# Kernel optimization log

Hardware: AMD Instinct MI355X
Metric: run time of the kernel (lower is better)

The kernel has to match this reference:

```python
import jax, jax.numpy as jnp
from jax import lax
import numpy as np


def hac_round(X, W):
    """Avg-linkage HAC build+cut rounding of fractional SDP matrix X (D,D).
    Returns the 0/1 symmetric round_matrix with 1-diagonal."""
    D = X.shape[0]
    dt = X.dtype
    MAXD = jnp.max(jnp.abs(X)) * 1000.0  # _MAX_DIST sentinel
    max_sim = jnp.max(X)                 # max_similarity passed by forward()
    tril_mask = jnp.tril(jnp.ones((D, D), dtype=bool))
    # use_similarities=True branch: Y = MAXD*tril + (max_sim - X).triu(1)
    Y = jnp.where(tril_mask, MAXD, max_sim - X)
    values = jnp.min(Y, axis=1)
    indices = jnp.argmin(Y, axis=1)
    parents = jnp.arange(2 * D - 1)
    p2i = jnp.arange(2 * D - 1)   # parent_to_idx
    i2p = jnp.arange(D)           # idx_to_parent
    cs = jnp.ones(2 * D - 1, dtype=dt)
    energy = jnp.zeros(2 * D - 1, dtype=dt)
    clustering = jnp.zeros((2 * D - 1, D), dtype=dt)
    clustering = clustering.at[jnp.arange(D), jnp.arange(D)].set(jnp.arange(1, D + 1, dtype=dt))
    R = jnp.eye(D, dtype=dt)

    def body(i, st):
        Y, values, indices, parents, p2i, i2p, cs, energy, clustering, R = st
        max_node = D + i
        m1 = jnp.argmin(values)
        m2 = indices[m1]
        p1 = i2p[p2i[i2p[m1]]]
        p2 = i2p[p2i[i2p[m2]]]
        parents = parents.at[p1].set(max_node).at[p2].set(max_node)
        i2p = i2p.at[m1].set(max_node)
        p2i = p2i.at[max_node].set(m1)
        max_mask = Y == MAXD
        cs1, cs2 = cs[p1], cs[p2]
        ncs = cs1 + cs2
        cs = cs.at[max_node].set(ncs)
        # weighted average-linkage merged distances
        newv = (jnp.minimum(Y[m1, :], Y[:, m1]) * cs1 + jnp.minimum(Y[:, m2], Y[m2, :]) * cs2) / ncs
        Y = Y.at[:, m1].set(newv).at[m1, :].set(newv)
        Y = jnp.where(max_mask, MAXD, Y)
        Y = Y.at[:, m2].set(MAXD).at[m2, :].set(MAXD)
        values = values.at[m2].set(MAXD)
        vmask = values == MAXD
        values = jnp.where(vmask, MAXD, jnp.min(Y, axis=1))
        indices = jnp.argmin(Y, axis=1)
        # cut decision for the new internal node
        crow = clustering[p1] + clustering[p2]
        leaf = crow > 0                      # membership of new cluster
        lf = leaf.astype(dt)
        merge_e = lf @ (W @ lf)              # sum of W over leaf x leaf pairs
        e_sum = energy[p1] + energy[p2]
        take = merge_e >= e_sum
        energy = energy.at[max_node].set(jnp.where(take, merge_e, e_sum))
        crow = jnp.where(take & leaf, (max_node).astype(dt), crow)
        clustering = clustering.at[max_node].set(crow)
        R = jnp.where(take & (leaf[:, None] & leaf[None, :]), jnp.asarray(1.0, dt), R)
        return (Y, values, indices, parents, p2i, i2p, cs, energy, clustering, R)

    st = (Y, values, indices, parents, p2i, i2p, cs, energy, clustering, R)
    st = lax.fori_loop(0, D - 1, body, st)
    return st[-1]


def setup_inputs() -> dict:
    key = jax.random.key(0)
    k1, k2 = jax.random.split(key)
    D = 1024
    A = jax.random.uniform(k1, (D, D), dtype=jnp.float32)
    X = 0.5 * (A + A.T)                      # symmetric fractional decisions
    X = X.at[jnp.arange(D), jnp.arange(D)].set(1.0)  # 1-diagonal
    W = jnp.triu(jax.random.normal(k2, (D, D), dtype=jnp.float32), 1)  # triu(1) weights
    return {"X": X, "W": W}


def reference(X, W):
    # straight-through estimator: hard rounded solution, identity gradient w.r.t. X
    R = hac_round(X, W)
    return X + lax.stop_gradient(R - X)
```

## Files before the change

### kernel.cpp

```cpp
#include <hip/hip_runtime.h>
#include <stdint.h>

#define D 1024

typedef unsigned long long u64;
typedef unsigned int u32;

__device__ __forceinline__ u32 enc_f(float f) {
    u32 b = __float_as_uint(f);
    return (b & 0x80000000u) ? ~b : (b | 0x80000000u);
}
__device__ __forceinline__ float dec_f(u32 u) {
    u32 b = (u & 0x80000000u) ? (u ^ 0x80000000u) : ~u;
    return __uint_as_float(b);
}

__device__ __forceinline__ void barrier_lds_only() {
    __builtin_amdgcn_sched_barrier(0);
    asm volatile("s_waitcnt lgkmcnt(0)" ::: "memory");
    __builtin_amdgcn_s_barrier();
    asm volatile("" ::: "memory");
    __builtin_amdgcn_sched_barrier(0);
}

__global__ void k_maxred(const float* __restrict__ X, u32* scal) {
    float mx = -INFINITY, ma = 0.f;
    int stride = gridDim.x * blockDim.x;
    for (int i = blockIdx.x * blockDim.x + threadIdx.x; i < D * D; i += stride) {
        float v = X[i];
        mx = fmaxf(mx, v);
        ma = fmaxf(ma, fabsf(v));
    }
    for (int o = 32; o; o >>= 1) {
        mx = fmaxf(mx, __shfl_xor(mx, o));
        ma = fmaxf(ma, __shfl_xor(ma, o));
    }
    if ((threadIdx.x & 63) == 0) {
        atomicMax(&scal[0], enc_f(mx));
        atomicMax(&scal[1], enc_f(ma));
    }
}

__global__ void k_init(const float* __restrict__ X, const float* __restrict__ W,
                       float2* __restrict__ dc, const u32* __restrict__ scal) {
    int idx = blockIdx.x * blockDim.x + threadIdx.x;
    if (idx >= D * D) return;
    float max_sim = dec_f(scal[0]);
    float MAXD = __fmul_rn(dec_f(scal[1]), 1000.0f);
    int i = idx >> 10, j = idx & (D - 1);
    float x = X[idx];
    float di = (i == j) ? MAXD : __fsub_rn(max_sim, x);
    float cx = (i == j) ? 0.0f : (W[idx] + W[j * D + i]);
    dc[idx] = make_float2(di, cx);
}

__global__ void k_rowmin(const float2* __restrict__ dc, float* __restrict__ values_g,
                         int* __restrict__ indices_g, const u32* __restrict__ scal) {
    int r = blockIdx.x;
    int lane = threadIdx.x;
    float MAXD = __fmul_rn(dec_f(scal[1]), 1000.0f);
    u64 best = ((u64)__float_as_uint(MAXD) << 32);
    const float4* row4 = (const float4*)(dc + (size_t)r * D);
    for (int c = lane; c < D / 2; c += 64) {
        float4 q = row4[c];
        int j0 = c << 1;
        if (j0 > r) {
            u64 k = ((u64)__float_as_uint(q.x) << 32) | (u32)j0;
            if (k < best) best = k;
        }
        if (j0 + 1 > r) {
            u64 k = ((u64)__float_as_uint(q.z) << 32) | (u32)(j0 + 1);
            if (k < best) best = k;
        }
    }
    for (int o = 32; o; o >>= 1) {
        u64 k2 = __shfl_xor(best, o);
        if (k2 < best) best = k2;
    }
    if (lane == 0) {
        values_g[r] = __uint_as_float((u32)(best >> 32));
        indices_g[r] = (int)(best & 0xffffffffu);
    }
}

__global__ void __launch_bounds__(1024) k_hac(
        float2* __restrict__ dc,
        const float* __restrict__ values_g, const int* __restrict__ indices_g,
        int* __restrict__ labels_g, const u32* __restrict__ scal) {
    __shared__ __align__(16) float values_l[D];
    __shared__ float values_stage[D];
    __shared__ int indices_l[D];
    __shared__ __align__(16) float newv_l[D];
    __shared__ float cs_l[D];
    __shared__ unsigned char dead_l[D];
    __shared__ unsigned char marked_l[D];
    __shared__ int slot_l[D];
    __shared__ int label_l[D];
    __shared__ double within_l[D];
    __shared__ double energy_l[D];
    __shared__ int rlist[2][D];
    __shared__ int nrec[2];
    __shared__ u64 s_best[2];
    __shared__ float s_cross12;
    __shared__ int s_takeP, s_m1P, s_labP;

    const int t = threadIdx.x;
    const int lane = t & 63, wid = t >> 6;
    const float MAXD = __fmul_rn(dec_f(scal[1]), 1000.0f);
    const u32 MAXDb = __float_as_uint(MAXD);

    values_l[t] = values_g[t];
    indices_l[t] = indices_g[t];
    cs_l[t] = 1.0f;
    dead_l[t] = 0;
    marked_l[t] = 0;
    slot_l[t] = t;
    label_l[t] = t;
    within_l[t] = 0.0;
    energy_l[t] = 0.0;
    if (t == 0) {
        s_takeP = 0; s_m1P = -1; s_labP = 0;
        nrec[0] = 0; nrec[1] = 0;
        s_best[0] = ~0ull; s_best[1] = ~0ull;
    }
    __syncthreads();
    {
        u64 key = ((u64)__float_as_uint(values_l[t]) << 32) | ((u32)t << 10) |
                  (u32)indices_l[t];
        for (int o = 32; o; o >>= 1) {
            u64 k2 = __shfl_xor(key, o);
            if (k2 < key) key = k2;
        }
        if (lane == 0) atomicMin(&s_best[0], key);
    }
    __syncthreads();

    float pf0 = 0.f, pf1 = 0.f, pf2 = 0.f, pf3 = 0.f;

    for (int it = 0; it < D - 1; ++it) {
        const int cb = it & 1, pb = cb ^ 1;

        const u64 bk = s_best[cb];
        const int m1 = (int)((bk >> 10) & 1023);
        const int m2 = (int)(bk & 1023);

        const float2 v1 = dc[(size_t)m1 * D + t];
        const float2 v2 = dc[(size_t)m2 * D + t];

        const float cs1 = cs_l[m1], cs2 = cs_l[m2];
        const float v_std = values_l[t];
        const float v_stg = values_stage[t];
        const int mk = marked_l[t];
        const int dd = dead_l[t];
        int idx = indices_l[t];
        const int sl = slot_l[t];
        const int pm1 = s_m1P;
        const int takeP = s_takeP, labP = s_labP;
        if (t == 0) s_best[pb] = ~0ull;

        const float ncs = __fadd_rn(cs1, cs2);

        float v = mk ? v_stg : v_std;
        if (mk) { values_l[t] = v; marked_l[t] = 0; }
        if (t == m2) {
            dead_l[m2] = 1;
            values_l[m2] = MAXD;
            indices_l[m2] = 0;
            v = MAXD;
            idx = 0;
        }
        const bool alive = !dd && (t != m2);

        const float d1 = v1.x, c1 = v1.y, d2 = v2.x, c2 = v2.y;

        if (takeP && sl == pm1) label_l[t] = labP;
        if (sl == m2) slot_l[t] = m1;

        float nv = MAXD, ncx = 0.0f;
        bool do_st = false;
        if (t == m2) s_cross12 = c1;
        if (alive && t != m1) {
            nv = __fdiv_rn(__fadd_rn(__fmul_rn(d1, cs1), __fmul_rn(d2, cs2)), ncs);
            ncx = c1 + c2;
            dc[(size_t)m1 * D + t] = make_float2(nv, ncx);
            do_st = true;
        }
        newv_l[t] = nv;

        if (t == m1) {
            values_l[t] = MAXD;
            marked_l[t] = 1;
        } else if (alive && v < MAXD) {
            if (idx == m2) {
                rlist[cb][atomicAdd(&nrec[cb], 1)] = t;
                values_l[t] = MAXD;
                marked_l[t] = 1;
            } else if (idx == m1) {
                if (nv <= v) values_l[t] = nv;
                else {
                    rlist[cb][atomicAdd(&nrec[cb], 1)] = t;
                    values_l[t] = MAXD;
                    marked_l[t] = 1;
                }
            } else if (t < m1) {
                if (nv < v) { values_l[t] = nv; indices_l[t] = m1; }
                else if (nv == v && m1 < idx) indices_l[t] = m1;
            }
        }
        barrier_lds_only();

        if (t == m1) cs_l[m1] = ncs;
        const int n = nrec[cb];
        if (t == 0) nrec[pb] = 0;

        if (wid == 0) {
            if (do_st) dc[(size_t)t * D + m1] = make_float2(nv, ncx);
            if (lane == 0) {
                double merge_e = within_l[m1] + within_l[m2] + (double)s_cross12;
                double e_sum = energy_l[m1] + energy_l[m2];
                int take = (merge_e >= e_sum) ? 1 : 0;
                within_l[m1] = merge_e;
                energy_l[m1] = take ? merge_e : e_sum;
                s_takeP = take;
                s_m1P = m1;
                s_labP = D + it;
            }
            const float4* v4 = (const float4*)values_l;
            u64 bb = ~0ull;
#pragma unroll
            for (int c = 0; c < 4; ++c) {
                int fi = lane + 64 * c;
                float4 q = v4[fi];
                int b = fi << 2;
                u64 k;
                k = ((u64)__float_as_uint(q.x) << 32) | (u32)(b + 0); if (k < bb) bb = k;
                k = ((u64)__float_as_uint(q.y) << 32) | (u32)(b + 1); if (k < bb) bb = k;
                k = ((u64)__float_as_uint(q.z) << 32) | (u32)(b + 2); if (k < bb) bb = k;
                k = ((u64)__float_as_uint(q.w) << 32) | (u32)(b + 3); if (k < bb) bb = k;
            }
            for (int o = 32; o; o >>= 1) {
                u64 k2 = __shfl_xor(bb, o);
                if (k2 < bb) bb = k2;
            }
            if (lane == 0) {
                int r = (int)(bb & 1023);
                int idx2 = indices_l[r];
                atomicMin(&s_best[pb],
                          (bb & 0xffffffff00000000ull) | ((u32)r << 10) | (u32)idx2);
            }
            {
                int r_pf = (int)(bb & 1023);
                int i_pf = indices_l[r_pf];
                const float* br = (const float*)(dc + (size_t)r_pf * D);
                const float* bi = (const float*)(dc + (size_t)i_pf * D);
                pf0 = br[lane * 16];
                pf1 = br[1024 + lane * 16];
                pf2 = bi[lane * 16];
                pf3 = bi[1024 + lane * 16];
            }
        } else if (wid == 1) {
            if (do_st) dc[(size_t)t * D + m1] = make_float2(nv, ncx);
            u64 bb = ((u64)MAXDb << 32);
            const float4* nv4 = (const float4*)newv_l;
            for (int c = lane; c < D / 4; c += 64) {
                float4 q = nv4[c];
                int j0 = c << 2;
#pragma unroll
                for (int e = 0; e < 4; ++e) {
                    int j = j0 + e;
                    float dv = (e == 0) ? q.x : (e == 1) ? q.y : (e == 2) ? q.z : q.w;
                    if (j > m1) {
                        u64 k = ((u64)__float_as_uint(dv) << 32) | (u32)j;
                        if (k < bb) bb = k;
                    }
                }
            }
            for (int o = 32; o; o >>= 1) {
                u64 k2 = __shfl_xor(bb, o);
                if (k2 < bb) bb = k2;
            }
            if (lane == 0) {
                values_stage[m1] = __uint_as_float((u32)(bb >> 32));
                indices_l[m1] = (int)(bb & 0xffffffffu);
                atomicMin(&s_best[pb],
                          (bb & 0xffffffff00000000ull) | ((u32)m1 << 10) | (bb & 1023));
            }
        } else {
            bool pend_st = do_st;
            for (int q = wid - 2; q < n; q += 14) {
                const int r = rlist[cb][q];
                const float subst = newv_l[r];
                const float4* row4 = (const float4*)(dc + (size_t)r * D);
                const int c0 = r >> 1;
                int ci0 = c0 + lane;       if (ci0 > 511) ci0 = 511;
                int ci1 = c0 + lane + 64;  if (ci1 > 511) ci1 = 511;
                int ci2 = c0 + lane + 128; if (ci2 > 511) ci2 = 511;
                int ci3 = c0 + lane + 192; if (ci3 > 511) ci3 = 511;
                int ci4 = c0 + lane + 256; if (ci4 > 511) ci4 = 511;
                int ci5 = c0 + lane + 320; if (ci5 > 511) ci5 = 511;
                int ci6 = c0 + lane + 384; if (ci6 > 511) ci6 = 511;
                int ci7 = c0 + lane + 448; if (ci7 > 511) ci7 = 511;
                float4 a0 = row4[ci0];
                float4 a1 = row4[ci1];
                float4 a2 = row4[ci2];
                float4 a3 = row4[ci3];
                float4 a4 = row4[ci4];
                float4 a5 = row4[ci5];
                float4 a6 = row4[ci6];
                float4 a7 = row4[ci7];
                if (pend_st) {
                    dc[(size_t)t * D + m1] = make_float2(nv, ncx);
                    pend_st = false;
                }
                u64 bb = ((u64)MAXDb << 32);
#define ACC2(af, civ)                                                           \
                {                                                               \
                    int j0 = (civ) << 1;                                        \
                    float dv0 = (j0 == m1) ? subst : (af).x;                    \
                    if (j0 > r && !dead_l[j0]) {                                \
                        u64 k = ((u64)__float_as_uint(dv0) << 32) | (u32)j0;    \
                        if (k < bb) bb = k;                                     \
                    }                                                           \
                    int j1 = j0 + 1;                                            \
                    float dv1 = (j1 == m1) ? subst : (af).z;                    \
                    if (j1 > r && !dead_l[j1]) {                                \
                        u64 k = ((u64)__float_as_uint(dv1) << 32) | (u32)j1;    \
                        if (k < bb) bb = k;                                     \
                    }                                                           \
                }
                ACC2(a0, ci0)
                ACC2(a1, ci1)
                ACC2(a2, ci2)
                ACC2(a3, ci3)
                ACC2(a4, ci4)
                ACC2(a5, ci5)
                ACC2(a6, ci6)
                ACC2(a7, ci7)
#undef ACC2
                for (int o = 32; o; o >>= 1) {
                    u64 k2 = __shfl_xor(bb, o);
                    if (k2 < bb) bb = k2;
                }
                if (lane == 0) {
                    values_stage[r] = __uint_as_float((u32)(bb >> 32));
                    indices_l[r] = (int)(bb & 0xffffffffu);
                    atomicMin(&s_best[pb],
                              (bb & 0xffffffff00000000ull) | ((u32)r << 10) | (bb & 1023));
                }
            }
            if (pend_st) dc[(size_t)t * D + m1] = make_float2(nv, ncx);
        }
        __syncthreads();
        if (wid == 0) asm volatile("" :: "v"(pf0), "v"(pf1), "v"(pf2), "v"(pf3));
    }

    {
        int lab = label_l[t];
        if (s_takeP && slot_l[t] == s_m1P) lab = s_labP;
        labels_g[t] = lab;
    }
}

__global__ void k_out(const int* __restrict__ labels, float* __restrict__ out) {
    int idx = blockIdx.x * blockDim.x + threadIdx.x;
    if (idx >= D * D) return;
    int i = idx >> 10, j = idx & (D - 1);
    out[idx] = (i == j || labels[i] == labels[j]) ? 1.0f : 0.0f;
}

extern "C" void kernel_launch(void* const* d_in, const int* in_sizes, int n_in,
                              void* d_out, int out_size, void* d_ws, size_t ws_size,
                              hipStream_t stream) {
    const float* X = (const float*)d_in[0];
    const float* W = (const float*)d_in[1];

    char* ws = (char*)d_ws;
    const size_t MAT_BYTES = (size_t)D * D * sizeof(float);
    float2* dc = (float2*)ws;
    float* values_g = (float*)(ws + 2 * MAT_BYTES);
    int* indices_g = (int*)(ws + 2 * MAT_BYTES + 4096);
    int* labels_g = (int*)(ws + 2 * MAT_BYTES + 8192);
    u32* scal = (u32*)(ws + 2 * MAT_BYTES + 12288);

    hipMemsetAsync(scal, 0, 2 * sizeof(u32), stream);
    k_maxred<<<256, 256, 0, stream>>>(X, scal);
    k_init<<<(D * D) / 256, 256, 0, stream>>>(X, W, dc, scal);
    k_rowmin<<<D, 64, 0, stream>>>(dc, values_g, indices_g, scal);
    k_hac<<<1, 1024, 0, stream>>>(dc, values_g, indices_g, labels_g, scal);
    k_out<<<(D * D) / 256, 256, 0, stream>>>(labels_g, (float*)d_out);
}
```

Measured before the change: 3.084 ms.

## Offload merged-row global stores to dedicated waves, forwarding values via LDS

Waves 0-7 now each process two columns of the merge update, and waves 8-15 do all the global writes of the merged row and column. The previous iteration's new row is double-buffered in LDS (newv_h/crossv_h), and readers of row m1/m2 take values from it when they touch the just-merged cluster. This lets the end-of-iteration `__syncthreads` become an LDS-only barrier, so store latency leaves the serial critical path. The cost is that row rescans now run on 6 waves instead of 14, and correctness depends on the store-visibility forwarding being exact.

```diff
diff --git a/kernel.cpp b/kernel.cpp
--- a/kernel.cpp
+++ b/kernel.cpp
@@ -90,7 +90,8 @@
     __shared__ __align__(16) float values_l[D];
     __shared__ float values_stage[D];
     __shared__ int indices_l[D];
-    __shared__ __align__(16) float newv_l[D];
+    __shared__ __align__(16) float newv_h[2][D];
+    __shared__ __align__(16) float crossv_h[2][D];
     __shared__ float cs_l[D];
     __shared__ unsigned char dead_l[D];
     __shared__ unsigned char marked_l[D];
@@ -143,214 +144,263 @@
         const u64 bk = s_best[cb];
         const int m1 = (int)((bk >> 10) & 1023);
         const int m2 = (int)(bk & 1023);
-
-        const float2 v1 = dc[(size_t)m1 * D + t];
-        const float2 v2 = dc[(size_t)m2 * D + t];
-
-        const float cs1 = cs_l[m1], cs2 = cs_l[m2];
-        const float v_std = values_l[t];
-        const float v_stg = values_stage[t];
-        const int mk = marked_l[t];
-        const int dd = dead_l[t];
-        int idx = indices_l[t];
-        const int sl = slot_l[t];
-        const int pm1 = s_m1P;
-        const int takeP = s_takeP, labP = s_labP;
-        if (t == 0) s_best[pb] = ~0ull;
-
-        const float ncs = __fadd_rn(cs1, cs2);
-
-        float v = mk ? v_stg : v_std;
-        if (mk) { values_l[t] = v; marked_l[t] = 0; }
-        if (t == m2) {
-            dead_l[m2] = 1;
-            values_l[m2] = MAXD;
-            indices_l[m2] = 0;
-            v = MAXD;
-            idx = 0;
-        }
-        const bool alive = !dd && (t != m2);
-
-        const float d1 = v1.x, c1 = v1.y, d2 = v2.x, c2 = v2.y;
-
-        if (takeP && sl == pm1) label_l[t] = labP;
-        if (sl == m2) slot_l[t] = m1;
-
-        float nv = MAXD, ncx = 0.0f;
-        bool do_st = false;
-        if (t == m2) s_cross12 = c1;
-        if (alive && t != m1) {
-            nv = __fdiv_rn(__fadd_rn(__fmul_rn(d1, cs1), __fmul_rn(d2, cs2)), ncs);
-            ncx = c1 + c2;
-            dc[(size_t)m1 * D + t] = make_float2(nv, ncx);
-            do_st = true;
-        }
-        newv_l[t] = nv;
-
-        if (t == m1) {
-            values_l[t] = MAXD;
-            marked_l[t] = 1;
-        } else if (alive && v < MAXD) {
-            if (idx == m2) {
-                rlist[cb][atomicAdd(&nrec[cb], 1)] = t;
-                values_l[t] = MAXD;
-                marked_l[t] = 1;
-            } else if (idx == m1) {
-                if (nv <= v) values_l[t] = nv;
-                else {
-                    rlist[cb][atomicAdd(&nrec[cb], 1)] = t;
-                    values_l[t] = MAXD;
-                    marked_l[t] = 1;
-                }
-            } else if (t < m1) {
-                if (nv < v) { values_l[t] = nv; indices_l[t] = m1; }
-                else if (nv == v && m1 < idx) indices_l[t] = m1;
-            }
+        const int c0 = (wid < 8) ? t : (t - 512);
+        const int c1 = c0 + 512;
+        float ncs = 0.f;
+
+        if (wid < 8) {
+            const float2 v1a = dc[(size_t)m1 * D + c0];
+            const float2 v1b = dc[(size_t)m1 * D + c1];
+            const float2 v2a = dc[(size_t)m2 * D + c0];
+            const float2 v2b = dc[(size_t)m2 * D + c1];
+
+            const int pm1 = s_m1P;
+            const float cs1 = cs_l[m1], cs2 = cs_l[m2];
+            float va = values_l[c0], vb = values_l[c1];
+            const float sga = values_stage[c0], sgb = values_stage[c1];
+            const int mka = marked_l[c0], mkb = marked_l[c1];
+            const int dda = dead_l[c0], ddb = dead_l[c1];
+            int ia = indices_l[c0], ib = indices_l[c1];
+            const int sla = slot_l[c0], slb = slot_l[c1];
+            const int takeP = s_takeP, labP = s_labP;
+            if (t == 0) s_best[pb] = ~0ull;
+
+            ncs = __fadd_rn(cs1, cs2);
+            const bool h1 = (m1 == pm1), h2 = (m2 == pm1);
+
+            if (mka) { va = sga; values_l[c0] = va; marked_l[c0] = 0; }
+            if (mkb) { vb = sgb; values_l[c1] = vb; marked_l[c1] = 0; }
+            if (c0 == m2) { dead_l[m2] = 1; values_l[m2] = MAXD; indices_l[m2] = 0; va = MAXD; ia = 0; }
+            if (c1 == m2) { dead_l[m2] = 1; values_l[m2] = MAXD; indices_l[m2] = 0; vb = MAXD; ib = 0; }
+            const bool alA = !dda && (c0 != m2);
+            const bool alB = !ddb && (c1 != m2);
+
+            float d1a = v1a.x, x1a = v1a.y, d1b = v1b.x, x1b = v1b.y;
+            float d2a = v2a.x, x2a = v2a.y, d2b = v2b.x, x2b = v2b.y;
+            if (h1) {
+                d1a = newv_h[pb][c0]; x1a = crossv_h[pb][c0];
+                d1b = newv_h[pb][c1]; x1b = crossv_h[pb][c1];
+            } else {
+                if (c0 == pm1) { d1a = newv_h[pb][m1]; x1a = crossv_h[pb][m1]; }
+                if (c1 == pm1) { d1b = newv_h[pb][m1]; x1b = crossv_h[pb][m1]; }
+            }
+            if (h2) {
+                d2a = newv_h[pb][c0]; x2a = crossv_h[pb][c0];
+                d2b = newv_h[pb][c1]; x2b = crossv_h[pb][c1];
+            } else {
+                if (c0 == pm1) { d2a = newv_h[pb][m2]; x2a = crossv_h[pb][m2]; }
+                if (c1 == pm1) { d2b = newv_h[pb][m2]; x2b = crossv_h[pb][m2]; }
+            }
+
+            if (takeP && sla == pm1) label_l[c0] = labP;
+            if (takeP && slb == pm1) label_l[c1] = labP;
+            if (sla == m2) slot_l[c0] = m1;
+            if (slb == m2) slot_l[c1] = m1;
+
+            if (c0 == m2) s_cross12 = x1a;
+            if (c1 == m2) s_cross12 = x1b;
+
+            float nva = MAXD, nxa = 0.0f, nvb = MAXD, nxb = 0.0f;
+            if (alA && c0 != m1) {
+                nva = __fdiv_rn(__fadd_rn(__fmul_rn(d1a, cs1), __fmul_rn(d2a, cs2)), ncs);
+                nxa = x1a + x2a;
+            }
+            if (alB && c1 != m1) {
+                nvb = __fdiv_rn(__fadd_rn(__fmul_rn(d1b, cs1), __fmul_rn(d2b, cs2)), ncs);
+                nxb = x1b + x2b;
+            }
+            newv_h[cb][c0] = nva; crossv_h[cb][c0] = nxa;
+            newv_h[cb][c1] = nvb; crossv_h[cb][c1] = nxb;
+
+            if (c0 == m1) {
+                values_l[c0] = MAXD;
+                marked_l[c0] = 1;
+            } else if (alA && va < MAXD) {
+                if (ia == m2) {
+                    rlist[cb][atomicAdd(&nrec[cb], 1)] = c0;
+                    values_l[c0] = MAXD; marked_l[c0] = 1;
+                } else if (ia == m1) {
+                    if (nva <= va) values_l[c0] = nva;
+                    else {
+                        rlist[cb][atomicAdd(&nrec[cb], 1)] = c0;
+                        values_l[c0] = MAXD; marked_l[c0] = 1;
+                    }
+                } else if (c0 < m1) {
+                    if (nva < va) { values_l[c0] = nva; indices_l[c0] = m1; }
+                    else if (nva == va && m1 < ia) indices_l[c0] = m1;
+                }
+            }
+            if (c1 == m1) {
+                values_l[c1] = MAXD;
+                marked_l[c1] = 1;
+            } else if (alB && vb < MAXD) {
+                if (ib == m2) {
+                    rlist[cb][atomicAdd(&nrec[cb], 1)] = c1;
+                    values_l[c1] = MAXD; marked_l[c1] = 1;
+                } else if (ib == m1) {
+                    if (nvb <= vb) values_l[c1] = nvb;
+                    else {
+                        rlist[cb][atomicAdd(&nrec[cb], 1)] = c1;
+                        values_l[c1] = MAXD; marked_l[c1] = 1;
+                    }
+                } else if (c1 < m1) {
+                    if (nvb < vb) { values_l[c1] = nvb; indices_l[c1] = m1; }
+                    else if (nvb == vb && m1 < ib) indices_l[c1] = m1;
+                }
+            }
+        } else {
+            asm volatile("s_waitcnt vmcnt(0)" ::: "memory");
         }
         barrier_lds_only();
 
-        if (t == m1) cs_l[m1] = ncs;
         const int n = nrec[cb];
         if (t == 0) nrec[pb] = 0;
 
-        if (wid == 0) {
-            if (do_st) dc[(size_t)t * D + m1] = make_float2(nv, ncx);
-            if (lane == 0) {
-                double merge_e = within_l[m1] + within_l[m2] + (double)s_cross12;
-                double e_sum = energy_l[m1] + energy_l[m2];
-                int take = (merge_e >= e_sum) ? 1 : 0;
-                within_l[m1] = merge_e;
-                energy_l[m1] = take ? merge_e : e_sum;
-                s_takeP = take;
-                s_m1P = m1;
-                s_labP = D + it;
-            }
-            const float4* v4 = (const float4*)values_l;
-            u64 bb = ~0ull;
+        if (wid < 8) {
+            if (c0 == m1 || c1 == m1) cs_l[m1] = ncs;
+
+            if (wid == 0) {
+                if (lane == 0) {
+                    double merge_e = within_l[m1] + within_l[m2] + (double)s_cross12;
+                    double e_sum = energy_l[m1] + energy_l[m2];
+                    int take = (merge_e >= e_sum) ? 1 : 0;
+                    within_l[m1] = merge_e;
+                    energy_l[m1] = take ? merge_e : e_sum;
+                    s_takeP = take;
+                    s_m1P = m1;
+                    s_labP = D + it;
+                }
+                const float4* v4 = (const float4*)values_l;
+                u64 bb = ~0ull;
 #pragma unroll
-            for (int c = 0; c < 4; ++c) {
-                int fi = lane + 64 * c;
-                float4 q = v4[fi];
-                int b = fi << 2;
-                u64 k;
-                k = ((u64)__float_as_uint(q.x) << 32) | (u32)(b + 0); if (k < bb) bb = k;
-                k = ((u64)__float_as_uint(q.y) << 32) | (u32)(b + 1); if (k < bb) bb = k;
-                k = ((u64)__float_as_uint(q.z) << 32) | (u32)(b + 2); if (k < bb) bb = k;
-                k = ((u64)__float_as_uint(q.w) << 32) | (u32)(b + 3); if (k < bb) bb = k;
-            }
-            for (int o = 32; o; o >>= 1) {
-                u64 k2 = __shfl_xor(bb, o);
-                if (k2 < bb) bb = k2;
-            }
-            if (lane == 0) {
-                int r = (int)(bb & 1023);
-                int idx2 = indices_l[r];
-                atomicMin(&s_best[pb],
-                          (bb & 0xffffffff00000000ull) | ((u32)r << 10) | (u32)idx2);
-            }
-            {
-                int r_pf = (int)(bb & 1023);
-                int i_pf = indices_l[r_pf];
-                const float* br = (const float*)(dc + (size_t)r_pf * D);
-                const float* bi = (const float*)(dc + (size_t)i_pf * D);
-                pf0 = br[lane * 16];
-                pf1 = br[1024 + lane * 16];
-                pf2 = bi[lane * 16];
-                pf3 = bi[1024 + lane * 16];
-            }
-        } else if (wid == 1) {
-            if (do_st) dc[(size_t)t * D + m1] = make_float2(nv, ncx);
-            u64 bb = ((u64)MAXDb << 32);
-            const float4* nv4 = (const float4*)newv_l;
-            for (int c = lane; c < D / 4; c += 64) {
-                float4 q = nv4[c];
-                int j0 = c << 2;
-#pragma unroll
-                for (int e = 0; e < 4; ++e) {
-                    int j = j0 + e;
-                    float dv = (e == 0) ? q.x : (e == 1) ? q.y : (e == 2) ? q.z : q.w;
-                    if (j > m1) {
-                        u64 k = ((u64)__float_as_uint(dv) << 32) | (u32)j;
-                        if (k < bb) bb = k;
-                    }
-                }
-            }
-            for (int o = 32; o; o >>= 1) {
-                u64 k2 = __shfl_xor(bb, o);
-                if (k2 < bb) bb = k2;
-            }
-            if (lane == 0) {
-                values_stage[m1] = __uint_as_float((u32)(bb >> 32));
-                indices_l[m1] = (int)(bb & 0xffffffffu);
-                atomicMin(&s_best[pb],
-                          (bb & 0xffffffff00000000ull) | ((u32)m1 << 10) | (bb & 1023));
-            }
-        } else {
-            bool pend_st = do_st;
-            for (int q = wid - 2; q < n; q += 14) {
-                const int r = rlist[cb][q];
-                const float subst = newv_l[r];
-                const float4* row4 = (const float4*)(dc + (size_t)r * D);
-                const int c0 = r >> 1;
-                int ci0 = c0 + lane;       if (ci0 > 511) ci0 = 511;
-                int ci1 = c0 + lane + 64;  if (ci1 > 511) ci1 = 511;
-                int ci2 = c0 + lane + 128; if (ci2 > 511) ci2 = 511;
-                int ci3 = c0 + lane + 192; if (ci3 > 511) ci3 = 511;
-                int ci4 = c0 + lane + 256; if (ci4 > 511) ci4 = 511;
-                int ci5 = c0 + lane + 320; if (ci5 > 511) ci5 = 511;
-                int ci6 = c0 + lane + 384; if (ci6 > 511) ci6 = 511;
-                int ci7 = c0 + lane + 448; if (ci7 > 511) ci7 = 511;
-                float4 a0 = row4[ci0];
-                float4 a1 = row4[ci1];
-                float4 a2 = row4[ci2];
-                float4 a3 = row4[ci3];
-                float4 a4 = row4[ci4];
-                float4 a5 = row4[ci5];
-                float4 a6 = row4[ci6];
-                float4 a7 = row4[ci7];
-                if (pend_st) {
-                    dc[(size_t)t * D + m1] = make_float2(nv, ncx);
-                    pend_st = false;
-                }
-                u64 bb = ((u64)MAXDb << 32);
-#define ACC2(af, civ)                                                           \
-                {                                                               \
-                    int j0 = (civ) << 1;                                        \
-                    float dv0 = (j0 == m1) ? subst : (af).x;                    \
-                    if (j0 > r && !dead_l[j0]) {                                \
-                        u64 k = ((u64)__float_as_uint(dv0) << 32) | (u32)j0;    \
-                        if (k < bb) bb = k;                                     \
-                    }                                                           \
-                    int j1 = j0 + 1;                                            \
-                    float dv1 = (j1 == m1) ? subst : (af).z;                    \
-                    if (j1 > r && !dead_l[j1]) {                                \
-                        u64 k = ((u64)__float_as_uint(dv1) << 32) | (u32)j1;    \
-                        if (k < bb) bb = k;                                     \
-                    }                                                           \
-                }
-                ACC2(a0, ci0)
-                ACC2(a1, ci1)
-                ACC2(a2, ci2)
-                ACC2(a3, ci3)
-                ACC2(a4, ci4)
-                ACC2(a5, ci5)
-                ACC2(a6, ci6)
-                ACC2(a7, ci7)
-#undef ACC2
+                for (int c = 0; c < 4; ++c) {
+                    int fi = lane + 64 * c;
+                    float4 q = v4[fi];
+                    int b = fi << 2;
+                    u64 k;
+                    k = ((u64)__float_as_uint(q.x) << 32) | (u32)(b + 0); if (k < bb) bb = k;
+                    k = ((u64)__float_as_uint(q.y) << 32) | (u32)(b + 1); if (k < bb) bb = k;
+                    k = ((u64)__float_as_uint(q.z) << 32) | (u32)(b + 2); if (k < bb) bb = k;
+                    k = ((u64)__float_as_uint(q.w) << 32) | (u32)(b + 3); if (k < bb) bb = k;
+                }
                 for (int o = 32; o; o >>= 1) {
                     u64 k2 = __shfl_xor(bb, o);
                     if (k2 < bb) bb = k2;
                 }
                 if (lane == 0) {
-                    values_stage[r] = __uint_as_float((u32)(bb >> 32));
-                    indices_l[r] = (int)(bb & 0xffffffffu);
+                    int r = (int)(bb & 1023);
+                    int idx2 = indices_l[r];
                     atomicMin(&s_best[pb],
-                              (bb & 0xffffffff00000000ull) | ((u32)r << 10) | (bb & 1023));
-                }
-            }
-            if (pend_st) dc[(size_t)t * D + m1] = make_float2(nv, ncx);
+                              (bb & 0xffffffff00000000ull) | ((u32)r << 10) | (u32)idx2);
+                }
+                {
+                    int r_pf = (int)(bb & 1023);
+                    int i_pf = indices_l[r_pf];
+                    const float* br = (const float*)(dc + (size_t)r_pf * D);
+                    const float* bi = (const float*)(dc + (size_t)i_pf * D);
+                    pf0 = br[lane * 16];
+                    pf1 = br[1024 + lane * 16];
+                    pf2 = bi[lane * 16];
+                    pf3 = bi[1024 + lane * 16];
+                }
+            } else if (wid == 1) {
+                u64 bb = ((u64)MAXDb << 32);
+                const float4* nv4 = (const float4*)newv_h[cb];
+                for (int c = lane; c < D / 4; c += 64) {
+                    float4 q = nv4[c];
+                    int j0 = c << 2;
+#pragma unroll
+                    for (int e = 0; e < 4; ++e) {
+                        int j = j0 + e;
+                        float dv = (e == 0) ? q.x : (e == 1) ? q.y : (e == 2) ? q.z : q.w;
+                        if (j > m1) {
+                            u64 k = ((u64)__float_as_uint(dv) << 32) | (u32)j;
+                            if (k < bb) bb = k;
+                        }
+                    }
+                }
+                for (int o = 32; o; o >>= 1) {
+                    u64 k2 = __shfl_xor(bb, o);
+                    if (k2 < bb) bb = k2;
+                }
+                if (lane == 0) {
+                    values_stage[m1] = __uint_as_float((u32)(bb >> 32));
+                    indices_l[m1] = (int)(bb & 0xffffffffu);
+                    atomicMin(&s_best[pb],
+                              (bb & 0xffffffff00000000ull) | ((u32)m1 << 10) | (bb & 1023));
+                }
+            } else {
+                for (int q = wid - 2; q < n; q += 6) {
+                    const int r = rlist[cb][q];
+                    const float subst = newv_h[cb][r];
+                    const float4* row4 = (const float4*)(dc + (size_t)r * D);
+                    const int cc0 = r >> 1;
+                    int ci0 = cc0 + lane;       if (ci0 > 511) ci0 = 511;
+                    int ci1 = cc0 + lane + 64;  if (ci1 > 511) ci1 = 511;
+                    int ci2 = cc0 + lane + 128; if (ci2 > 511) ci2 = 511;
+                    int ci3 = cc0 + lane + 192; if (ci3 > 511) ci3 = 511;
+                    int ci4 = cc0 + lane + 256; if (ci4 > 511) ci4 = 511;
+                    int ci5 = cc0 + lane + 320; if (ci5 > 511) ci5 = 511;
+                    int ci6 = cc0 + lane + 384; if (ci6 > 511) ci6 = 511;
+                    int ci7 = cc0 + lane + 448; if (ci7 > 511) ci7 = 511;
+                    float4 a0 = row4[ci0];
+                    float4 a1 = row4[ci1];
+                    float4 a2 = row4[ci2];
+                    float4 a3 = row4[ci3];
+                    float4 a4 = row4[ci4];
+                    float4 a5 = row4[ci5];
+                    float4 a6 = row4[ci6];
+                    float4 a7 = row4[ci7];
+                    u64 bb = ((u64)MAXDb << 32);
+#define ACC2(af, civ)                                                           \
+                    {                                                           \
+                        int j0 = (civ) << 1;                                    \
+                        float dv0 = (j0 == m1) ? subst : (af).x;                \
+                        if (j0 > r && !dead_l[j0]) {                            \
+                            u64 k = ((u64)__float_as_uint(dv0) << 32) | (u32)j0;\
+                            if (k < bb) bb = k;                                 \
+                        }                                                       \
+                        int j1 = j0 + 1;                                        \
+                        float dv1 = (j1 == m1) ? subst : (af).z;                \
+                        if (j1 > r && !dead_l[j1]) {                            \
+                            u64 k = ((u64)__float_as_uint(dv1) << 32) | (u32)j1;\
+                            if (k < bb) bb = k;                                 \
+                        }                                                       \
+                    }
+                    ACC2(a0, ci0)
+                    ACC2(a1, ci1)
+                    ACC2(a2, ci2)
+                    ACC2(a3, ci3)
+                    ACC2(a4, ci4)
+                    ACC2(a5, ci5)
+                    ACC2(a6, ci6)
+                    ACC2(a7, ci7)
+#undef ACC2
+                    for (int o = 32; o; o >>= 1) {
+                        u64 k2 = __shfl_xor(bb, o);
+                        if (k2 < bb) bb = k2;
+                    }
+                    if (lane == 0) {
+                        values_stage[r] = __uint_as_float((u32)(bb >> 32));
+                        indices_l[r] = (int)(bb & 0xffffffffu);
+                        atomicMin(&s_best[pb],
+                                  (bb & 0xffffffff00000000ull) | ((u32)r << 10) | (bb & 1023));
+                    }
+                }
+            }
+        } else {
+            const float nva = newv_h[cb][c0], nxa = crossv_h[cb][c0];
+            const float nvb = newv_h[cb][c1], nxb = crossv_h[cb][c1];
+            if (nva != MAXD) {
+                dc[(size_t)m1 * D + c0] = make_float2(nva, nxa);
+                dc[(size_t)c0 * D + m1] = make_float2(nva, nxa);
+            }
+            if (nvb != MAXD) {
+                dc[(size_t)m1 * D + c1] = make_float2(nvb, nxb);
+                dc[(size_t)c1 * D + m1] = make_float2(nvb, nxb);
+            }
         }
-        __syncthreads();
+        barrier_lds_only();
         if (wid == 0) asm volatile("" :: "v"(pf0), "v"(pf1), "v"(pf2), "v"(pf3));
     }
 
```

New measurement: 4.207 ms. 36.4% more time.
